# Kernel optimization log

Measured on AMD Instinct MI355X. Metric: run time of the kernel, lower is better.

The kernel has to match this reference:

```python
import jax, jax.numpy as jnp
import numpy as np

STRIDES = [4, 8, 16, 32, 64]
SIZES = [32.0, 64.0, 128.0, 256.0, 512.0]
RATIOS = [0.5, 1.0, 2.0]
IMG = 1024.0
PRE_NMS = 1000
POST_NMS = 1000
NMS_THR = 0.7
MIN_SIZE = 0.0
SCALE_CLAMP = float(np.log(1000.0 / 16.0))
NEG = -1e4  # finite sentinel instead of -inf (keeps grads clean)


def conv(x, w, b, pad):
    y = jax.lax.conv_general_dilated(x, w, (1, 1), pad,
                                     dimension_numbers=('NCHW', 'OIHW', 'NCHW'))
    return y + b[None, :, None, None]


def gen_anchors(H, W, stride, size):
    # detectron2 cell anchors: w = size/sqrt(r), h = w*r, centered at shift
    rs = jnp.asarray(RATIOS, jnp.float32)
    ws = size / jnp.sqrt(rs)
    hs = ws * rs
    base = jnp.stack([-ws / 2, -hs / 2, ws / 2, hs / 2], -1)  # [A,4]
    sx = jnp.arange(W, dtype=jnp.float32) * stride
    sy = jnp.arange(H, dtype=jnp.float32) * stride
    shy, shx = jnp.meshgrid(sy, sx, indexing='ij')
    shifts = jnp.stack([shx, shy, shx, shy], -1)  # [H,W,4]
    return (shifts[:, :, None, :] + base[None, None]).reshape(-1, 4)  # [H*W*A,4]


def apply_deltas(d, boxes):
    # Box2BoxTransform.apply_deltas with weights (1,1,1,1)
    w = boxes[..., 2] - boxes[..., 0]
    h = boxes[..., 3] - boxes[..., 1]
    cx = boxes[..., 0] + 0.5 * w
    cy = boxes[..., 1] + 0.5 * h
    dx, dy = d[..., 0], d[..., 1]
    dw = jnp.minimum(d[..., 2], SCALE_CLAMP)
    dh = jnp.minimum(d[..., 3], SCALE_CLAMP)
    pcx = dx * w + cx
    pcy = dy * h + cy
    pw = jnp.exp(dw) * w
    ph = jnp.exp(dh) * h
    return jnp.stack([pcx - 0.5 * pw, pcy - 0.5 * ph,
                      pcx + 0.5 * pw, pcy + 0.5 * ph], -1)


def pairwise_iou(b):
    area = (b[:, 2] - b[:, 0]) * (b[:, 3] - b[:, 1])
    lt = jnp.maximum(b[:, None, :2], b[None, :, :2])
    rb = jnp.minimum(b[:, None, 2:], b[None, :, 2:])
    wh = jnp.clip(rb - lt, 0.0)
    inter = wh[..., 0] * wh[..., 1]
    return inter / (area[:, None] + area[None, :] - inter + 1e-9)


def nms_single(boxes, off_boxes, scores, valid):
    # greedy NMS over score-sorted candidates; off_boxes carry per-level offsets
    order = jnp.argsort(-scores)
    b = boxes[order]
    ob = off_boxes[order]
    s = scores[order]
    v = valid[order]
    M = b.shape[0]
    iou = pairwise_iou(ob)
    sup = (iou > NMS_THR) & jnp.tril(jnp.ones((M, M), bool), -1)

    def step(keep, xs):
        row, vi, i = xs
        ki = vi & jnp.logical_not(jnp.any(keep & row))
        return keep.at[i].set(ki), None

    keep, _ = jax.lax.scan(step, jnp.zeros((M,), bool), (sup, v, jnp.arange(M)))
    ks = jnp.where(keep, s, NEG)
    topv, topi = jax.lax.top_k(ks, POST_NMS)
    return b[topi], topv


def rpn_forward(feats, w_conv, b_conv, w_obj, b_obj, w_delta, b_delta):
    scores, boxes, lvls = [], [], []
    for lvl, (f, st, sz) in enumerate(zip(feats, STRIDES, SIZES)):
        t = jax.nn.relu(conv(f, w_conv, b_conv, 'SAME'))
        logit = conv(t, w_obj, b_obj, 'VALID')   # [N,A,H,W]
        delta = conv(t, w_delta, b_delta, 'VALID')  # [N,4A,H,W]
        N, A, H, W = logit.shape
        logit = logit.transpose(0, 2, 3, 1).reshape(N, H * W * A)
        delta = delta.reshape(N, A, 4, H, W).transpose(0, 3, 4, 1, 2).reshape(N, H * W * A, 4)
        anch = gen_anchors(H, W, st, sz)
        k = min(PRE_NMS, H * W * A)
        ts, ti = jax.lax.top_k(logit, k)  # per-level pre-NMS topk
        td = jnp.take_along_axis(delta, ti[..., None], axis=1)
        ta = anch[ti]
        scores.append(ts)
        boxes.append(apply_deltas(td, ta))
        lvls.append(jnp.full((k,), float(lvl), jnp.float32))
    s = jnp.concatenate(scores, 1)                 # [N, M]
    b = jnp.concatenate(boxes, 1)                  # [N, M, 4]
    l = jnp.concatenate(lvls)                      # [M]
    b = jnp.clip(b, 0.0, IMG)                      # clip to image
    bw = b[..., 2] - b[..., 0]
    bh = b[..., 3] - b[..., 1]
    valid = (bw > MIN_SIZE) & (bh > MIN_SIZE)      # min-size filter as mask
    ob = b + (l * (IMG * 4.0))[None, :, None]      # batched_nms level offsets
    nb, ns = jax.vmap(nms_single, in_axes=(0, 0, 0, 0))(b, ob, s, valid)
    return jnp.concatenate([nb, ns[..., None]], -1)  # [N, POST_NMS, 5]


def setup_inputs() -> dict:
    key = jax.random.key(0)
    ks = jax.random.split(key, 8)
    inp = {
        'feat0': jax.random.normal(ks[0], (2, 256, 256, 256), jnp.float32),
        'feat1': jax.random.normal(ks[1], (2, 256, 128, 128), jnp.float32),
        'feat2': jax.random.normal(ks[2], (2, 256, 64, 64), jnp.float32),
        'feat3': jax.random.normal(ks[3], (2, 256, 32, 32), jnp.float32),
        'feat4': jax.random.normal(ks[4], (2, 256, 16, 16), jnp.float32),
        'w_conv': jax.random.normal(ks[5], (256, 256, 3, 3), jnp.float32) * 0.02,
        'b_conv': jnp.zeros((256,), jnp.float32),
        'w_obj': jax.random.normal(ks[6], (3, 256, 1, 1), jnp.float32) * 0.05,
        'b_obj': jnp.zeros((3,), jnp.float32),
        'w_delta': jax.random.normal(ks[7], (12, 256, 1, 1), jnp.float32) * 0.05,
        'b_delta': jnp.zeros((12,), jnp.float32),
    }
    return inp


def reference(feat0, feat1, feat2, feat3, feat4, w_conv, b_conv, w_obj, b_obj, w_delta, b_delta):
    return rpn_forward([feat0, feat1, feat2, feat3, feat4],
                       w_conv, b_conv, w_obj, b_obj, w_delta, b_delta)
```

## Files before the change

### kernel.cpp

```cpp
#include <hip/hip_runtime.h>
#include <cstdint>
#include <cstddef>

static constexpr int NIMG = 2;
static constexpr int CCH  = 256;
static constexpr int LTOT = 261888;
static constexpr int MCAT = 4768;
static constexpr int MW   = 75;
static constexpr double SCALE_CLAMP_D = 4.135166556742356;


__device__ __forceinline__ unsigned keyd(float f) {
  unsigned u = __float_as_uint(f);
  return (u >> 31) ? ~u : (u | 0x80000000u);
}
__device__ __forceinline__ float invkey(unsigned d) {
  unsigned u = (d & 0x80000000u) ? (d & 0x7FFFFFFFu) : ~d;
  return __uint_as_float(u);
}

__global__ void k_wT(const float* __restrict__ w, float* __restrict__ wT) {
  int i = blockIdx.x * 256 + threadIdx.x;
  if (i >= 2304 * 256) return;
  int co = i & 255;
  int ct = i >> 8;
  wT[ct * 256 + co] = w[co * 2304 + ct];
}

__device__ __forceinline__ void conv_body(
    const float* __restrict__ x, const float* __restrict__ wT,
    const float* __restrict__ bias, float* __restrict__ t,
    int H, int W, int n, int cog, int h0, int w0) {
  __shared__ __align__(16) float xs[8][6][76];
  __shared__ __align__(16) float wsm[8][9][64];
  const int cout0 = cog * 64;
  const int tx = threadIdx.x;
  const int cog4 = tx >> 4;
  const int pxg  = tx & 15;
  const int r2   = pxg >> 2;
  const int col0 = (pxg & 3) * 16;

  float acc[4][16];
#pragma unroll
  for (int a = 0; a < 4; ++a)
#pragma unroll
    for (int b = 0; b < 16; ++b) acc[a][b] = 0.f;

  for (int ck = 0; ck < 32; ++ck) {
#pragma unroll
    for (int ci = 0; ci < 8; ++ci) {
      const float* xc = x + (size_t)(n * CCH + ck * 8 + ci) * H * W;
      for (int e = tx; e < 396; e += 256) {
        int r = e / 66, c = e - r * 66;
        int gh = h0 - 1 + r, gw = w0 - 1 + c;
        float v = 0.f;
        if ((unsigned)gh < (unsigned)H && (unsigned)gw < (unsigned)W)
          v = xc[gh * W + gw];
        xs[ci][r][c] = v;
      }
    }
#pragma unroll
    for (int ci = 0; ci < 8; ++ci) {
      for (int e = tx; e < 576; e += 256) {
        int tap = e >> 6, co = e & 63;
        wsm[ci][tap][co] = wT[((size_t)(ck * 8 + ci) * 9 + tap) * 256 + cout0 + co];
      }
    }
    __syncthreads();

#pragma unroll
    for (int ci = 0; ci < 8; ++ci) {
#pragma unroll
      for (int kh = 0; kh < 3; ++kh) {
        const float* p = &xs[ci][r2 + kh][col0];
        float4 a0 = *reinterpret_cast<const float4*>(p);
        float4 a1 = *reinterpret_cast<const float4*>(p + 4);
        float4 a2 = *reinterpret_cast<const float4*>(p + 8);
        float4 a3 = *reinterpret_cast<const float4*>(p + 12);
        float2 a4 = *reinterpret_cast<const float2*>(p + 16);
        float xr[18] = {a0.x, a0.y, a0.z, a0.w, a1.x, a1.y, a1.z, a1.w,
                        a2.x, a2.y, a2.z, a2.w, a3.x, a3.y, a3.z, a3.w,
                        a4.x, a4.y};
#pragma unroll
        for (int kw = 0; kw < 3; ++kw) {
          float4 wq = *reinterpret_cast<const float4*>(&wsm[ci][kh * 3 + kw][cog4 * 4]);
          float wv[4] = {wq.x, wq.y, wq.z, wq.w};
#pragma unroll
          for (int co = 0; co < 4; ++co)
#pragma unroll
            for (int j = 0; j < 16; ++j)
              acc[co][j] = fmaf(xr[j + kw], wv[co], acc[co][j]);
        }
      }
    }
    __syncthreads();
  }

  const int h = h0 + r2;
#pragma unroll
  for (int co = 0; co < 4; ++co) {
    int c = cout0 + cog4 * 4 + co;
    float bv = bias[c];
#pragma unroll
    for (int j = 0; j < 16; ++j) {
      int ww = w0 + col0 + j;
      if (ww < W) {
        float v = acc[co][j] + bv;
        t[((size_t)(n * CCH + c) * H + h) * W + ww] = v > 0.f ? v : 0.f;
      }
    }
  }
}

__global__ __launch_bounds__(256, 3)
void k_conv0(const float* __restrict__ x, const float* __restrict__ wT,
             const float* __restrict__ bias, float* __restrict__ t) {
  int n = blockIdx.z >> 2, cog = blockIdx.z & 3;
  conv_body(x, wT, bias, t, 256, 256, n, cog, blockIdx.y * 4, blockIdx.x * 64);
}

__global__ __launch_bounds__(256, 3)
void k_conv4(const float* __restrict__ f1, const float* __restrict__ f2,
             const float* __restrict__ f3, const float* __restrict__ f4,
             const float* __restrict__ wT, const float* __restrict__ bias,
             float* __restrict__ t) {
  int b = blockIdx.x;
  const float* x; float* tb; int H, gx, gy, l;
  if (b < 512)      { x = f1; tb = t;            H = 128; gx = 2; gy = 32; l = b; }
  else if (b < 640) { x = f2; tb = t +  8388608; H =  64; gx = 1; gy = 16; l = b - 512; }
  else if (b < 704) { x = f3; tb = t + 10485760; H =  32; gx = 1; gy =  8; l = b - 640; }
  else              { x = f4; tb = t + 11010048; H =  16; gx = 1; gy =  4; l = b - 704; }
  int bx = l % gx;
  int by = (l / gx) % gy;
  int bz = l / (gx * gy);
  int n = bz >> 2, cog = bz & 3;
  conv_body(x, wT, bias, tb, H, H, n, cog, by * 4, bx * 64);
}

__device__ __forceinline__ void heads_body(
    const float* __restrict__ t,
    const float* __restrict__ wobj, const float* __restrict__ bobj,
    const float* __restrict__ wdel, const float* __restrict__ bdel,
    float* __restrict__ logits, float4* __restrict__ deltas,
    int HW, int loff, int n, int p0) {
  __shared__ float wl[15][256];
  __shared__ float bl[15];
  for (int i = threadIdx.x; i < 15 * 256; i += 256) {
    int o = i >> 8, c = i & 255;
    wl[o][c] = (o < 3) ? wobj[o * 256 + c] : wdel[(o - 3) * 256 + c];
  }
  if (threadIdx.x < 15)
    bl[threadIdx.x] = (threadIdx.x < 3) ? bobj[threadIdx.x] : bdel[threadIdx.x - 3];
  __syncthreads();
  if (p0 >= HW) return;

  float4 acc[15];
#pragma unroll
  for (int o = 0; o < 15; ++o) acc[o] = make_float4(0.f, 0.f, 0.f, 0.f);
  const float* tp = t + (size_t)n * CCH * HW + p0;
  for (int c = 0; c < 256; ++c) {
    float4 v = *reinterpret_cast<const float4*>(tp + (size_t)c * HW);
#pragma unroll
    for (int o = 0; o < 15; ++o) {
      float wv = wl[o][c];
      acc[o].x = fmaf(v.x, wv, acc[o].x);
      acc[o].y = fmaf(v.y, wv, acc[o].y);
      acc[o].z = fmaf(v.z, wv, acc[o].z);
      acc[o].w = fmaf(v.w, wv, acc[o].w);
    }
  }
#pragma unroll
  for (int o = 0; o < 15; ++o) {
    float bv = bl[o];
    acc[o].x += bv; acc[o].y += bv; acc[o].z += bv; acc[o].w += bv;
  }

  const float* af = reinterpret_cast<const float*>(acc);
  size_t base = (size_t)n * LTOT + loff + (size_t)p0 * 3;
#pragma unroll
  for (int i2 = 0; i2 < 4; ++i2) {
#pragma unroll
    for (int a = 0; a < 3; ++a) {
      logits[base + i2 * 3 + a] = af[a * 4 + i2];
      deltas[base + i2 * 3 + a] =
          make_float4(af[(3 + a * 4 + 0) * 4 + i2], af[(3 + a * 4 + 1) * 4 + i2],
                      af[(3 + a * 4 + 2) * 4 + i2], af[(3 + a * 4 + 3) * 4 + i2]);
    }
  }
}

__global__ __launch_bounds__(256)
void k_heads0(const float* __restrict__ t,
              const float* __restrict__ wobj, const float* __restrict__ bobj,
              const float* __restrict__ wdel, const float* __restrict__ bdel,
              float* __restrict__ logits, float4* __restrict__ deltas) {
  heads_body(t, wobj, bobj, wdel, bdel, logits, deltas,
             65536, 0, blockIdx.y, (blockIdx.x * 256 + threadIdx.x) * 4);
}

__global__ __launch_bounds__(256)
void k_heads4(const float* __restrict__ t,
              const float* __restrict__ wobj, const float* __restrict__ bobj,
              const float* __restrict__ wdel, const float* __restrict__ bdel,
              float* __restrict__ logits, float4* __restrict__ deltas) {
  int b = blockIdx.x;
  const float* tb; int HW, loff, start;
  if (b < 16)      { tb = t;            HW = 16384; loff = 196608; start = 0;  }
  else if (b < 20) { tb = t +  8388608; HW =  4096; loff = 245760; start = 16; }
  else if (b < 21) { tb = t + 10485760; HW =  1024; loff = 258048; start = 20; }
  else             { tb = t + 11010048; HW =   256; loff = 261120; start = 21; }
  heads_body(tb, wobj, bobj, wdel, bdel, logits, deltas,
             HW, loff, blockIdx.y, ((b - start) * 256 + threadIdx.x) * 4);
}

__global__ __launch_bounds__(1024)
void k_topk(const float* __restrict__ logits, const float4* __restrict__ deltas,
            float* __restrict__ scat, float4* __restrict__ bout,
            double* __restrict__ obout, unsigned* __restrict__ valid) {
  constexpr int   Hs[5]    = {256, 128, 64, 32, 16};
  constexpr int   strd[5]  = {4, 8, 16, 32, 64};
  constexpr float szs[5]   = {32.f, 64.f, 128.f, 256.f, 512.f};
  constexpr int   loffs[5] = {0, 196608, 245760, 258048, 261120};
  constexpr int   Ms[5]    = {196608, 49152, 12288, 3072, 768};
  constexpr int   ksz[5]   = {1000, 1000, 1000, 1000, 768};
  constexpr int   coffs[5] = {0, 1000, 2000, 3000, 4000};

  __shared__ unsigned hist[2048];
  __shared__ unsigned long long cand[1024];
  __shared__ unsigned tie[1024];
  __shared__ unsigned sB1, sC1, sB2, sC2, sDK, sTN;
  __shared__ unsigned cntG, cntT;

  const int task = blockIdx.x;
  const int n = task / 5, lvl = task % 5;
  const int M = Ms[lvl], K = ksz[lvl], loff = loffs[lvl];
  const float* lg = logits + (size_t)n * LTOT + loff;
  const int tid = threadIdx.x;

  for (int i = tid; i < 2048; i += 1024) hist[i] = 0;
  if (tid == 0) { cntG = 0; cntT = 0; }
  __syncthreads();
  for (int i = tid; i < M; i += 1024) atomicAdd(&hist[keyd(lg[i]) >> 21], 1u);
  __syncthreads();
  if (tid == 0) {
    unsigned acc = 0;
    for (int b = 2047; b >= 0; --b) {
      unsigned na = acc + hist[b];
      if (na >= (unsigned)K) { sB1 = (unsigned)b; sC1 = acc; break; }
      acc = na;
    }
  }
  __syncthreads();
  const unsigned B1 = sB1;
  const unsigned rem1 = (unsigned)K - sC1;

  for (int i = tid; i < 2048; i += 1024) hist[i] = 0;
  __syncthreads();
  for (int i = tid; i < M; i += 1024) {
    unsigned d = keyd(lg[i]);
    if ((d >> 21) == B1) atomicAdd(&hist[(d >> 10) & 0x7FFu], 1u);
  }
  __syncthreads();
  if (tid == 0) {
    unsigned acc = 0;
    for (int b = 2047; b >= 0; --b) {
      unsigned na = acc + hist[b];
      if (na >= rem1) { sB2 = (unsigned)b; sC2 = acc; break; }
      acc = na;
    }
  }
  __syncthreads();
  const unsigned B2 = sB2;
  const unsigned rem2 = rem1 - sC2;
  const unsigned pfx = (B1 << 11) | B2;

  for (int i = tid; i < 1024; i += 1024) hist[i] = 0;
  __syncthreads();
  for (int i = tid; i < M; i += 1024) {
    unsigned d = keyd(lg[i]);
    if ((d >> 10) == pfx) atomicAdd(&hist[d & 0x3FFu], 1u);
  }
  __syncthreads();
  if (tid == 0) {
    unsigned acc = 0;
    for (int b = 1023; b >= 0; --b) {
      unsigned na = acc + hist[b];
      if (na >= rem2) { sDK = (pfx << 10) | (unsigned)b; sTN = rem2 - acc; break; }
      acc = na;
    }
  }
  __syncthreads();
  const unsigned dk = sDK;
  const unsigned tneed = sTN;
  const unsigned cg = (unsigned)K - tneed;

  for (int i = tid; i < M; i += 1024) {
    unsigned d = keyd(lg[i]);
    if (d > dk) {
      unsigned p = atomicAdd(&cntG, 1u);
      cand[p] = ((unsigned long long)(~d) << 32) | (unsigned)i;
    } else if (d == dk) {
      unsigned q = atomicAdd(&cntT, 1u);
      if (q < 1024u) tie[q] = (unsigned)i;
    }
  }
  __syncthreads();
  if (tid == 0) {
    int ct = (int)(cntT < 1024u ? cntT : 1024u);
    for (int a = 1; a < ct; ++a) {
      unsigned v = tie[a]; int b = a - 1;
      while (b >= 0 && tie[b] > v) { tie[b + 1] = tie[b]; --b; }
      tie[b + 1] = v;
    }
    for (unsigned q = 0; q < tneed; ++q)
      cand[cg + q] = ((unsigned long long)(~dk) << 32) | tie[q];
  }
  __syncthreads();
  if (tid >= K) cand[tid] = ~0ULL;
  __syncthreads();

  for (unsigned k2 = 2; k2 <= 1024; k2 <<= 1)
    for (unsigned j = k2 >> 1; j > 0; j >>= 1) {
      __syncthreads();
      unsigned i = (unsigned)tid, l = i ^ j;
      if (l > i) {
        unsigned long long a = cand[i], b = cand[l];
        bool up = ((i & k2) == 0);
        if (up ? (a > b) : (a < b)) { cand[i] = b; cand[l] = a; }
      }
    }
  __syncthreads();

  if (tid < K) {
    unsigned long long kk = cand[tid];
    unsigned idx = (unsigned)kk;
    unsigned d = ~(unsigned)(kk >> 32);
    float s = invkey(d);
    int catpos = n * MCAT + coffs[lvl] + tid;
    scat[catpos] = s;

    int a = idx % 3;
    int pix = idx / 3;
    int W = Hs[lvl];
    int hh = pix / W;
    int ww = pix - hh * W;
    float4 d4 = deltas[(size_t)n * LTOT + loff + idx];

    double r  = (a == 0) ? 0.5 : (a == 1 ? 1.0 : 2.0);
    double sz = (double)szs[lvl];
    double cw = sz / sqrt(r);
    double ch = cw * r;
    double cx = (double)(ww * strd[lvl]);
    double cy = (double)(hh * strd[lvl]);
    double dx = (double)d4.x, dy = (double)d4.y;
    double dw = (double)d4.z; if (dw > SCALE_CLAMP_D) dw = SCALE_CLAMP_D;
    double dh = (double)d4.w; if (dh > SCALE_CLAMP_D) dh = SCALE_CLAMP_D;
    double pcx = dx * cw + cx, pcy = dy * ch + cy;
    double pw = exp(dw) * cw,  ph = exp(dh) * ch;
    double x0 = pcx - 0.5 * pw, y0 = pcy - 0.5 * ph;
    double x1 = pcx + 0.5 * pw, y1 = pcy + 0.5 * ph;
    x0 = x0 < 0.0 ? 0.0 : (x0 > 1024.0 ? 1024.0 : x0);
    y0 = y0 < 0.0 ? 0.0 : (y0 > 1024.0 ? 1024.0 : y0);
    x1 = x1 < 0.0 ? 0.0 : (x1 > 1024.0 ? 1024.0 : x1);
    y1 = y1 < 0.0 ? 0.0 : (y1 > 1024.0 ? 1024.0 : y1);
    bool vld = ((x1 - x0) > 0.0) && ((y1 - y0) > 0.0);

    bout[catpos] = make_float4((float)x0, (float)y0, (float)x1, (float)y1);
    double off = (double)lvl * 4096.0;
    double* op = obout + (size_t)catpos * 4;
    op[0] = x0 + off; op[1] = y0 + off; op[2] = x1 + off; op[3] = y1 + off;
    valid[catpos] = vld ? 1u : 0u;
  }
}

__global__ __launch_bounds__(1024)
void k_sort(const float* __restrict__ scat, const float4* __restrict__ b,
            const double* __restrict__ ob, const unsigned* __restrict__ valid,
            float* __restrict__ s_s, float4* __restrict__ b_s,
            double* __restrict__ ob_s, unsigned* __restrict__ valid_s) {
  __shared__ unsigned long long sk[8192];
  const int n = blockIdx.x;
  const int tid = threadIdx.x;
  for (int i = tid; i < 8192; i += 1024)
    sk[i] = (i < MCAT)
      ? ((unsigned long long)(~keyd(scat[n * MCAT + i])) << 32) | (unsigned)i
      : ~0ULL;
  __syncthreads();
  for (unsigned k2 = 2; k2 <= 8192; k2 <<= 1)
    for (unsigned j = k2 >> 1; j > 0; j >>= 1) {
      for (int m = 0; m < 8; ++m) {
        unsigned i = (unsigned)tid + (unsigned)m * 1024u;
        unsigned l = i ^ j;
        if (l > i) {
          unsigned long long a = sk[i], bb = sk[l];
          bool up = ((i & k2) == 0);
          if (up ? (a > bb) : (a < bb)) { sk[i] = bb; sk[l] = a; }
        }
      }
      __syncthreads();
    }
  for (int r = tid; r < MCAT; r += 1024) {
    unsigned long long kk = sk[r];
    unsigned pos = (unsigned)kk;
    unsigned d = ~(unsigned)(kk >> 32);
    s_s[n * MCAT + r] = invkey(d);
    b_s[n * MCAT + r] = b[n * MCAT + pos];
    const double* src = ob + ((size_t)n * MCAT + pos) * 4;
    double* dst = ob_s + ((size_t)n * MCAT + r) * 4;
    dst[0] = src[0]; dst[1] = src[1]; dst[2] = src[2]; dst[3] = src[3];
    valid_s[n * MCAT + r] = valid[n * MCAT + pos];
  }
}

__global__ __launch_bounds__(256)
void k_mask(const double* __restrict__ ob_s, unsigned long long* __restrict__ mask) {
  const int n = blockIdx.y;
  const int i = blockIdx.x;
  const double* bi = ob_s + ((size_t)n * MCAT + i) * 4;
  const double ix0 = bi[0], iy0 = bi[1], ix1 = bi[2], iy1 = bi[3];
  const double ai = (ix1 - ix0) * (iy1 - iy0);
  const int tid = threadIdx.x;
  for (int j0 = 0; j0 < MCAT; j0 += 256) {
    int j = j0 + tid;
    bool sup = false;
    if (j < MCAT && j > i) {
      const double* bj = ob_s + ((size_t)n * MCAT + j) * 4;
      double jx0 = bj[0], jy0 = bj[1], jx1 = bj[2], jy1 = bj[3];
      double aj = (jx1 - jx0) * (jy1 - jy0);
      double lx = ix0 > jx0 ? ix0 : jx0;
      double ly = iy0 > jy0 ? iy0 : jy0;
      double rx = ix1 < jx1 ? ix1 : jx1;
      double ry = iy1 < jy1 ? iy1 : jy1;
      double wx = rx - lx; wx = wx > 0.0 ? wx : 0.0;
      double wy = ry - ly; wy = wy > 0.0 ? wy : 0.0;
      double inter = wx * wy;
      double iou = inter / (ai + aj - inter + 1e-9);
      sup = iou > 0.7;
    }
    unsigned long long bal = __ballot(sup);
    if ((tid & 63) == 0) {
      int word = (j0 + tid) >> 6;
      if (word < MW) mask[((size_t)n * MCAT + i) * MW + word] = bal;
    }
  }
}

__global__ __launch_bounds__(256)
void k_nms(const unsigned long long* __restrict__ mask,
           const unsigned* __restrict__ valid_s,
           const float* __restrict__ s_s, const float4* __restrict__ b_s,
           float* __restrict__ out) {
  __shared__ unsigned long long rem[MW];
  __shared__ unsigned long long supcc[64];
  __shared__ unsigned long long keepw[MW];
  __shared__ int kl[64];
  __shared__ int snk;
  __shared__ unsigned kpfx[MW], nkpfx[MW];
  __shared__ unsigned sKept;
  const int n = blockIdx.x;
  const int tid = threadIdx.x;
  const unsigned long long* msk = mask + (size_t)n * MCAT * MW;

  for (int w = tid; w < MW; w += 256) {
    unsigned long long r = 0ULL;
    for (int b = 0; b < 64; ++b) {
      int i = w * 64 + b;
      bool rm = (i >= MCAT) || (valid_s[n * MCAT + i] == 0u);
      if (rm) r |= (1ULL << b);
    }
    rem[w] = r;
    keepw[w] = 0ULL;
  }
  __syncthreads();

  for (int c = 0; c < MW; ++c) {
    if (tid < 64) {
      int i = c * 64 + tid;
      supcc[tid] = (i < MCAT) ? msk[(size_t)i * MW + c] : 0ULL;
    }
    __syncthreads();
    if (tid == 0) {
      unsigned long long r = rem[c], km = 0ULL;
      int nk = 0;
      for (int b = 0; b < 64; ++b) {
        if (!((r >> b) & 1ULL)) { km |= (1ULL << b); kl[nk++] = b; r |= supcc[b]; }
      }
      rem[c] = r; keepw[c] = km; snk = nk;
    }
    __syncthreads();
    const int nk = snk;
    const int nw = MW - 1 - c;
    const int total = nk * nw;
    for (int idx = tid; idx < total; idx += 256) {
      int b = kl[idx / nw];
      int w = c + 1 + (idx % nw);
      unsigned long long v = msk[(size_t)(c * 64 + b) * MW + w];
      if (v) atomicOr(&rem[w], v);
    }
    __syncthreads();
  }

  if (tid == 0) {
    unsigned ka = 0, na = 0;
    for (int w = 0; w < MW; ++w) {
      kpfx[w] = ka; nkpfx[w] = na;
      unsigned long long range = (w < MW - 1) ? ~0ULL : ((1ULL << 32) - 1ULL);
      ka += (unsigned)__popcll(keepw[w]);
      na += (unsigned)__popcll((~keepw[w]) & range);
    }
    sKept = ka;
  }
  __syncthreads();
  const unsigned keptTotal = sKept;

  for (int i = tid; i < MCAT; i += 256) {
    int w = i >> 6, b = i & 63;
    unsigned long long below = (1ULL << b) - 1ULL;
    bool kept = (keepw[w] >> b) & 1ULL;
    unsigned row;
    if (kept)
      row = kpfx[w] + (unsigned)__popcll(keepw[w] & below);
    else
      row = keptTotal + nkpfx[w] + (unsigned)__popcll((~keepw[w]) & below);
    if (row < 1000u) {
      float4 bb = b_s[n * MCAT + i];
      float sc = kept ? s_s[n * MCAT + i] : -1e4f;
      float* o = out + ((size_t)n * 1000 + row) * 5;
      o[0] = bb.x; o[1] = bb.y; o[2] = bb.z; o[3] = bb.w; o[4] = sc;
    }
  }
}

extern "C" void kernel_launch(void* const* d_in, const int* in_sizes, int n_in,
                              void* d_out, int out_size, void* d_ws, size_t ws_size,
                              hipStream_t stream) {
  (void)in_sizes; (void)n_in; (void)out_size;
  const float* feats[5] = {(const float*)d_in[0], (const float*)d_in[1],
                           (const float*)d_in[2], (const float*)d_in[3],
                           (const float*)d_in[4]};
  const float* w_conv = (const float*)d_in[5];
  const float* b_conv = (const float*)d_in[6];
  const float* w_obj  = (const float*)d_in[7];
  const float* b_obj  = (const float*)d_in[8];
  const float* w_del  = (const float*)d_in[9];
  const float* b_del  = (const float*)d_in[10];
  float* out = (float*)d_out;

  char* p = (char*)d_ws;
  auto alloc = [&](size_t bytes) -> void* {
    void* r = (void*)p;
    p += (bytes + 255) & ~(size_t)255;
    return r;
  };
  float*  t       = (float*)  alloc((size_t)2 * 256 * 256 * 256 * 4);
  float*  wT      = (float*)  alloc((size_t)2304 * 256 * 4);
  float*  logits  = (float*)  alloc((size_t)NIMG * LTOT * 4);
  float4* deltas  = (float4*) alloc((size_t)NIMG * LTOT * 16);
  float*  scat    = (float*)  alloc((size_t)NIMG * MCAT * 4);
  float4* bout    = (float4*) alloc((size_t)NIMG * MCAT * 16);
  double* obout   = (double*) alloc((size_t)NIMG * MCAT * 32);
  unsigned* valid = (unsigned*)alloc((size_t)NIMG * MCAT * 4);
  float*  s_s     = (float*)  alloc((size_t)NIMG * MCAT * 4);
  float4* b_s     = (float4*) alloc((size_t)NIMG * MCAT * 16);
  double* ob_s    = (double*) alloc((size_t)NIMG * MCAT * 32);
  unsigned* val_s = (unsigned*)alloc((size_t)NIMG * MCAT * 4);
  unsigned long long* mask =
      (unsigned long long*)alloc((size_t)NIMG * MCAT * MW * 8);
  if ((size_t)(p - (char*)d_ws) > ws_size) return;

  k_wT<<<2304, 256, 0, stream>>>(w_conv, wT);

  k_conv4<<<736, 256, 0, stream>>>(feats[1], feats[2], feats[3], feats[4],
                                   wT, b_conv, t);
  k_heads4<<<dim3(22, 2), 256, 0, stream>>>(t, w_obj, b_obj, w_del, b_del,
                                            logits, deltas);
  k_conv0<<<dim3(4, 64, 8), 256, 0, stream>>>(feats[0], wT, b_conv, t);
  k_heads0<<<dim3(64, 2), 256, 0, stream>>>(t, w_obj, b_obj, w_del, b_del,
                                            logits, deltas);

  k_topk<<<10, 1024, 0, stream>>>(logits, deltas, scat, bout, obout, valid);
  k_sort<<<2, 1024, 0, stream>>>(scat, bout, obout, valid, s_s, b_s, ob_s, val_s);
  k_mask<<<dim3(MCAT, 2), 256, 0, stream>>>(ob_s, mask);
  k_nms<<<2, 256, 0, stream>>>(mask, val_s, s_s, b_s, out);
}
```

Before: 4.562 ms.

## Double-buffer conv input and weight tiles in LDS with precomputed offsets

Splits the shared-memory input and weight tiles into two buffers so the next channel chunk is staged while the current one is computed, removing one barrier per iteration. Per-thread halo load offsets and validity are precomputed once, replacing per-iteration division and bounds checks. The doubled LDS footprint forces launch bounds down from three to two blocks per CU, trading occupancy for overlap.

```diff
diff --git a/kernel.cpp b/kernel.cpp
--- a/kernel.cpp
+++ b/kernel.cpp
@@ -31,14 +31,52 @@
     const float* __restrict__ x, const float* __restrict__ wT,
     const float* __restrict__ bias, float* __restrict__ t,
     int H, int W, int n, int cog, int h0, int w0) {
-  __shared__ __align__(16) float xs[8][6][76];
-  __shared__ __align__(16) float wsm[8][9][64];
+  __shared__ __align__(16) float xs[2][8][6][68];
+  __shared__ __align__(16) float wsm[2][8][9][64];
+
   const int cout0 = cog * 64;
   const int tx = threadIdx.x;
   const int cog4 = tx >> 4;
   const int pxg  = tx & 15;
   const int r2   = pxg >> 2;
   const int col0 = (pxg & 3) * 16;
+  const int HWi  = H * W;
+
+  const int ra = tx / 66, ca = tx - ra * 66;
+  const int e1 = tx + 256;
+  const int rb = e1 / 66, cb = e1 - rb * 66;
+  const int gha = h0 - 1 + ra, gwa = w0 - 1 + ca;
+  const int ghb = h0 - 1 + rb, gwb = w0 - 1 + cb;
+  const bool va = (unsigned)gha < (unsigned)H && (unsigned)gwa < (unsigned)W;
+  const bool vb = (tx < 140) && (unsigned)ghb < (unsigned)H &&
+                  (unsigned)gwb < (unsigned)W;
+  const int offa = va ? (gha * W + gwa) : 0;
+  const int offb = vb ? (ghb * W + gwb) : 0;
+  const float* xb = x + (size_t)n * CCH * HWi;
+
+  const int tapA = tx >> 6, coA = tx & 63;
+
+  auto stage = [&](int ck, int bi) {
+    const float* xk = xb + (size_t)ck * 8 * HWi;
+#pragma unroll
+    for (int ci = 0; ci < 8; ++ci) {
+      const float* xc = xk + ci * HWi;
+      float u0 = xc[offa];
+      xs[bi][ci][ra][ca] = va ? u0 : 0.f;
+      if (tx < 140) {
+        float u1 = xc[offb];
+        xs[bi][ci][rb][cb] = vb ? u1 : 0.f;
+      }
+    }
+    const float* wk = wT + (size_t)(ck * 8) * 9 * 256 + cout0;
+#pragma unroll
+    for (int ci = 0; ci < 8; ++ci) {
+      const float* wc = wk + (size_t)ci * 9 * 256;
+      wsm[bi][ci][tapA][coA]     = wc[tapA * 256 + coA];
+      wsm[bi][ci][4 + tapA][coA] = wc[(4 + tapA) * 256 + coA];
+      if (tx < 64) wsm[bi][ci][8][tx] = wc[8 * 256 + tx];
+    }
+  };
 
   float acc[4][16];
 #pragma unroll
@@ -46,33 +84,18 @@
 #pragma unroll
     for (int b = 0; b < 16; ++b) acc[a][b] = 0.f;
 
+  stage(0, 0);
+  __syncthreads();
+
   for (int ck = 0; ck < 32; ++ck) {
+    const int cur = ck & 1;
+    if (ck < 31) stage(ck + 1, cur ^ 1);
+
 #pragma unroll
     for (int ci = 0; ci < 8; ++ci) {
-      const float* xc = x + (size_t)(n * CCH + ck * 8 + ci) * H * W;
-      for (int e = tx; e < 396; e += 256) {
-        int r = e / 66, c = e - r * 66;
-        int gh = h0 - 1 + r, gw = w0 - 1 + c;
-        float v = 0.f;
-        if ((unsigned)gh < (unsigned)H && (unsigned)gw < (unsigned)W)
-          v = xc[gh * W + gw];
-        xs[ci][r][c] = v;
-      }
-    }
-#pragma unroll
-    for (int ci = 0; ci < 8; ++ci) {
-      for (int e = tx; e < 576; e += 256) {
-        int tap = e >> 6, co = e & 63;
-        wsm[ci][tap][co] = wT[((size_t)(ck * 8 + ci) * 9 + tap) * 256 + cout0 + co];
-      }
-    }
-    __syncthreads();
-
-#pragma unroll
-    for (int ci = 0; ci < 8; ++ci) {
 #pragma unroll
       for (int kh = 0; kh < 3; ++kh) {
-        const float* p = &xs[ci][r2 + kh][col0];
+        const float* p = &xs[cur][ci][r2 + kh][col0];
         float4 a0 = *reinterpret_cast<const float4*>(p);
         float4 a1 = *reinterpret_cast<const float4*>(p + 4);
         float4 a2 = *reinterpret_cast<const float4*>(p + 8);
@@ -83,7 +106,8 @@
                         a4.x, a4.y};
 #pragma unroll
         for (int kw = 0; kw < 3; ++kw) {
-          float4 wq = *reinterpret_cast<const float4*>(&wsm[ci][kh * 3 + kw][cog4 * 4]);
+          float4 wq = *reinterpret_cast<const float4*>(
+              &wsm[cur][ci][kh * 3 + kw][cog4 * 4]);
           float wv[4] = {wq.x, wq.y, wq.z, wq.w};
 #pragma unroll
           for (int co = 0; co < 4; ++co)
@@ -112,14 +136,14 @@
   }
 }
 
-__global__ __launch_bounds__(256, 3)
+__global__ __launch_bounds__(256, 2)
 void k_conv0(const float* __restrict__ x, const float* __restrict__ wT,
              const float* __restrict__ bias, float* __restrict__ t) {
   int n = blockIdx.z >> 2, cog = blockIdx.z & 3;
   conv_body(x, wT, bias, t, 256, 256, n, cog, blockIdx.y * 4, blockIdx.x * 64);
 }
 
-__global__ __launch_bounds__(256, 3)
+__global__ __launch_bounds__(256, 2)
 void k_conv4(const float* __restrict__ f1, const float* __restrict__ f2,
              const float* __restrict__ f3, const float* __restrict__ f4,
              const float* __restrict__ wT, const float* __restrict__ bias,
```

New measurement: 4.768 ms. 4.5% more time.

## Retile 3x3 conv: 16-row input tiles, 512 threads, weights read per-wave from global

Applied to the files above, without the earlier changes.

The conv kernel now uses 512-thread blocks that each cover 16 output rows and 32 output channels, up from 4 rows and 64 channels. The input tile grows to 18 rows, so the halo overhead per output drops and each staged input is reused across more rows. Weights are no longer staged in shared memory; each wave reads its float4 weights straight from global memory (wave-uniform, so they can be served by scalar or cached loads), which removes one staging pass. In exchange, each input tile is now loaded by eight channel-group blocks instead of four, the grid has fewer blocks, and register pressure rises under the 512-thread, 4-block launch bound.

```diff
diff --git a/kernel.cpp b/kernel.cpp
--- a/kernel.cpp
+++ b/kernel.cpp
@@ -30,15 +30,31 @@
 __device__ __forceinline__ void conv_body(
     const float* __restrict__ x, const float* __restrict__ wT,
     const float* __restrict__ bias, float* __restrict__ t,
-    int H, int W, int n, int cog, int h0, int w0) {
-  __shared__ __align__(16) float xs[8][6][76];
-  __shared__ __align__(16) float wsm[8][9][64];
-  const int cout0 = cog * 64;
-  const int tx = threadIdx.x;
-  const int cog4 = tx >> 4;
-  const int pxg  = tx & 15;
-  const int r2   = pxg >> 2;
-  const int col0 = (pxg & 3) * 16;
+    int H, int W, int n, int cog8, int h0, int w0) {
+  __shared__ __align__(16) float xs[8][18][68];
+
+  const int tx   = threadIdx.x;
+  const int wid  = __builtin_amdgcn_readfirstlane(tx >> 6);
+  const int lane = tx & 63;
+  const int r    = lane >> 2;
+  const int col0 = (lane & 3) * 16;
+  const int HWi  = H * W;
+
+  int sra[3], sca[3], soffa[3]; bool sva[3];
+#pragma unroll
+  for (int k = 0; k < 3; ++k) {
+    int e = tx + k * 512;
+    int rr = e / 66, cc = e - rr * 66;
+    sra[k] = rr; sca[k] = cc;
+    int gh = h0 - 1 + rr, gw = w0 - 1 + cc;
+    bool v = (e < 1188) && ((unsigned)gh < (unsigned)H) &&
+             ((unsigned)gw < (unsigned)W);
+    sva[k] = v;
+    soffa[k] = v ? (gh * W + gw) : 0;
+  }
+  const float* xb = x + (size_t)n * CCH * HWi;
+
+  const float* wbase = wT + cog8 * 32 + wid * 4;
 
   float acc[4][16];
 #pragma unroll
@@ -47,32 +63,27 @@
     for (int b = 0; b < 16; ++b) acc[a][b] = 0.f;
 
   for (int ck = 0; ck < 32; ++ck) {
+    __syncthreads();
 #pragma unroll
     for (int ci = 0; ci < 8; ++ci) {
-      const float* xc = x + (size_t)(n * CCH + ck * 8 + ci) * H * W;
-      for (int e = tx; e < 396; e += 256) {
-        int r = e / 66, c = e - r * 66;
-        int gh = h0 - 1 + r, gw = w0 - 1 + c;
-        float v = 0.f;
-        if ((unsigned)gh < (unsigned)H && (unsigned)gw < (unsigned)W)
-          v = xc[gh * W + gw];
-        xs[ci][r][c] = v;
+      const float* xc = xb + (size_t)(ck * 8 + ci) * HWi;
+#pragma unroll
+      for (int k = 0; k < 3; ++k) {
+        if (k < 2 || tx < 164) {
+          float u = xc[soffa[k]];
+          xs[ci][sra[k]][sca[k]] = sva[k] ? u : 0.f;
+        }
       }
     }
+    __syncthreads();
+
+    const float* wck = wbase + (size_t)(ck * 8) * 9 * 256;
 #pragma unroll
     for (int ci = 0; ci < 8; ++ci) {
-      for (int e = tx; e < 576; e += 256) {
-        int tap = e >> 6, co = e & 63;
-        wsm[ci][tap][co] = wT[((size_t)(ck * 8 + ci) * 9 + tap) * 256 + cout0 + co];
-      }
-    }
-    __syncthreads();
-
-#pragma unroll
-    for (int ci = 0; ci < 8; ++ci) {
+      const float* wc = wck + (size_t)ci * 9 * 256;
 #pragma unroll
       for (int kh = 0; kh < 3; ++kh) {
-        const float* p = &xs[ci][r2 + kh][col0];
+        const float* p = &xs[ci][r + kh][col0];
         float4 a0 = *reinterpret_cast<const float4*>(p);
         float4 a1 = *reinterpret_cast<const float4*>(p + 4);
         float4 a2 = *reinterpret_cast<const float4*>(p + 8);
@@ -83,7 +94,7 @@
                         a4.x, a4.y};
 #pragma unroll
         for (int kw = 0; kw < 3; ++kw) {
-          float4 wq = *reinterpret_cast<const float4*>(&wsm[ci][kh * 3 + kw][cog4 * 4]);
+          float4 wq = *reinterpret_cast<const float4*>(wc + (kh * 3 + kw) * 256);
           float wv[4] = {wq.x, wq.y, wq.z, wq.w};
 #pragma unroll
           for (int co = 0; co < 4; ++co)
@@ -93,13 +104,12 @@
         }
       }
     }
-    __syncthreads();
-  }
-
-  const int h = h0 + r2;
+  }
+
+  const int h = h0 + r;
 #pragma unroll
   for (int co = 0; co < 4; ++co) {
-    int c = cout0 + cog4 * 4 + co;
+    int c = cog8 * 32 + wid * 4 + co;
     float bv = bias[c];
 #pragma unroll
     for (int j = 0; j < 16; ++j) {
@@ -112,29 +122,31 @@
   }
 }
 
-__global__ __launch_bounds__(256, 3)
+__global__ __launch_bounds__(512, 4)
 void k_conv0(const float* __restrict__ x, const float* __restrict__ wT,
              const float* __restrict__ bias, float* __restrict__ t) {
-  int n = blockIdx.z >> 2, cog = blockIdx.z & 3;
-  conv_body(x, wT, bias, t, 256, 256, n, cog, blockIdx.y * 4, blockIdx.x * 64);
-}
-
-__global__ __launch_bounds__(256, 3)
+  int bz = blockIdx.z;
+  int n = bz >> 3, cog8 = bz & 7;
+  conv_body(x, wT, bias, t, 256, 256, n, cog8, blockIdx.y * 16, blockIdx.x * 64);
+}
+
+__global__ __launch_bounds__(512, 4)
 void k_conv4(const float* __restrict__ f1, const float* __restrict__ f2,
              const float* __restrict__ f3, const float* __restrict__ f4,
              const float* __restrict__ wT, const float* __restrict__ bias,
              float* __restrict__ t) {
   int b = blockIdx.x;
-  const float* x; float* tb; int H, gx, gy, l;
-  if (b < 512)      { x = f1; tb = t;            H = 128; gx = 2; gy = 32; l = b; }
-  else if (b < 640) { x = f2; tb = t +  8388608; H =  64; gx = 1; gy = 16; l = b - 512; }
-  else if (b < 704) { x = f3; tb = t + 10485760; H =  32; gx = 1; gy =  8; l = b - 640; }
-  else              { x = f4; tb = t + 11010048; H =  16; gx = 1; gy =  4; l = b - 704; }
-  int bx = l % gx;
-  int by = (l / gx) % gy;
-  int bz = l / (gx * gy);
-  int n = bz >> 2, cog = bz & 3;
-  conv_body(x, wT, bias, tb, H, H, n, cog, by * 4, bx * 64);
+  const float* x; float* tb; int H, l, bx, by, bz;
+  if (b < 256)      { x = f1; tb = t;            H = 128; l = b;
+                      bx = l & 1; by = (l >> 1) & 7; bz = l >> 4; }
+  else if (b < 320) { x = f2; tb = t +  8388608; H =  64; l = b - 256;
+                      bx = 0;     by = l & 3;        bz = l >> 2; }
+  else if (b < 352) { x = f3; tb = t + 10485760; H =  32; l = b - 320;
+                      bx = 0;     by = l & 1;        bz = l >> 1; }
+  else              { x = f4; tb = t + 11010048; H =  16; l = b - 352;
+                      bx = 0;     by = 0;            bz = l; }
+  int n = bz >> 3, cog8 = bz & 7;
+  conv_body(x, wT, bias, tb, H, H, n, cog8, by * 16, bx * 64);
 }
 
 __device__ __forceinline__ void heads_body(
@@ -570,11 +582,11 @@
 
   k_wT<<<2304, 256, 0, stream>>>(w_conv, wT);
 
-  k_conv4<<<736, 256, 0, stream>>>(feats[1], feats[2], feats[3], feats[4],
+  k_conv4<<<368, 512, 0, stream>>>(feats[1], feats[2], feats[3], feats[4],
                                    wT, b_conv, t);
   k_heads4<<<dim3(22, 2), 256, 0, stream>>>(t, w_obj, b_obj, w_del, b_del,
                                             logits, deltas);
-  k_conv0<<<dim3(4, 64, 8), 256, 0, stream>>>(feats[0], wT, b_conv, t);
+  k_conv0<<<dim3(4, 16, 16), 512, 0, stream>>>(feats[0], wT, b_conv, t);
   k_heads0<<<dim3(64, 2), 256, 0, stream>>>(t, w_obj, b_obj, w_del, b_del,
                                             logits, deltas);
 
```

After: 5.189 ms. 13.7% more time.
